# Kernel optimization log

Measured on AMD Instinct MI355X. Metric: run time of the kernel, lower is better.

Reference implementation:

```python
import jax, jax.numpy as jnp
import numpy as np

N = 262144      # nodes
E = 1048576     # edges
NC = 30         # node feature dim
ED = 13         # bond (edge) feature dim
H = 256         # hidden_channels
GH = 512        # config.gnn_hidden_channels
OUT = 256       # out_channels
L = 4           # num_layers
G = 8192        # num graphs in batch


def setup_inputs() -> dict:
    key = jax.random.key(0)
    ks = jax.random.split(key, 16)
    inp = {
        "x": jax.random.normal(ks[0], (N, NC), jnp.float32),
        "edge_attr": jax.random.normal(ks[1], (E, ED), jnp.float32),
        "edge_index": jax.random.randint(ks[2], (2, E), 0, N, jnp.int64),
        "batch": jnp.sort(jax.random.randint(ks[3], (N,), 0, G, jnp.int64)),
        # node_to_hid: Linear(NC, H)
        "W_nh": jax.random.normal(ks[4], (NC, H), jnp.float32) / np.sqrt(NC),
        "b_nh": jnp.zeros((H,), jnp.float32),
        # shared GINEConv nn: Linear(H, H) + ReLU (same module instance for every layer)
        "W1": jax.random.normal(ks[5], (H, H), jnp.float32) / np.sqrt(H),
        "b1": jnp.zeros((H,), jnp.float32),
        # per-layer edge projection Linear(ED, H) inside each GINEConv
        "We": jax.random.normal(ks[6], (L, ED, H), jnp.float32) / np.sqrt(ED),
        "be": jnp.zeros((L, H), jnp.float32),
        # lin1: H -> GH, lin2: GH -> OUT
        "Wl1": jax.random.normal(ks[7], (H, GH), jnp.float32) / np.sqrt(H),
        "bl1": jnp.zeros((GH,), jnp.float32),
        "Wl2": jax.random.normal(ks[8], (GH, OUT), jnp.float32) / np.sqrt(GH),
        "bl2": jnp.zeros((OUT,), jnp.float32),
    }
    return inp


def reference(x, edge_attr, W_nh, b_nh, W1, b1, We, be, Wl1, bl1, Wl2, bl2,
              edge_index, batch):
    src = edge_index[0]  # x_j (messages flow source -> target)
    dst = edge_index[1]
    hid = x @ W_nh + b_nh                                   # [N, H]
    for l in range(L):
        e = edge_attr @ We[l] + be[l]                       # [E, H]
        msg = jax.nn.relu(hid[src] + e)                     # gather + fuse
        agg = jax.ops.segment_sum(msg, dst, num_segments=N) # scatter-sum
        # GINEConv (eps=0) -> shared nn (Linear+ReLU), then outer relu in forward
        hid = jax.nn.relu(jax.nn.relu((hid + agg) @ W1 + b1))
    out = jax.nn.relu(hid @ Wl1 + bl1) @ Wl2 + bl2          # [N, OUT]
    # global_add_pool readout
    return jax.ops.segment_sum(out, batch, num_segments=G)  # [G, OUT]
```

## Files before the change

### kernel.cpp

```cpp
#include <hip/hip_runtime.h>
#include <hip/hip_bf16.h>

#define N_NODES 262144
#define N_EDGES 1048576
#define NC      30
#define ED      13
#define H       256
#define GH      512
#define OUT_C   256
#define NLAYERS 4
#define NGRAPHS 8192

typedef __hip_bfloat16 bf16;
typedef __attribute__((ext_vector_type(8))) short short8;
typedef __attribute__((ext_vector_type(4))) float f32x4;

__device__ unsigned short g_W1t[H * H];
__device__ unsigned short g_Wl1t[2][H * H];
__device__ unsigned short g_Wl2t[2][H * H];
__device__ float g_b1[H];
__device__ float g_bl1[GH];
__device__ float g_bl2[OUT_C];
__device__ unsigned int g_ssrc[N_EDGES];
__device__ float        g_seat[N_EDGES * ED];
__device__ unsigned int g_rowptr[N_NODES + 1];
__device__ unsigned int g_cursor[N_NODES];
__device__ unsigned int g_bsum[1024];

__device__ __forceinline__ float hw2f(unsigned short h) {
    return __uint_as_float(((unsigned int)h) << 16);
}
__device__ __forceinline__ float ldf(const void* p, size_t i, bool isbf) {
    return isbf ? hw2f(((const unsigned short*)p)[i]) : ((const float*)p)[i];
}
__device__ __forceinline__ int ldi(const void* p, size_t j, bool is64) {
    return ((const int*)p)[is64 ? 2 * j : j];
}
__device__ __forceinline__ unsigned short bfbits(float f) {
    bf16 b = __float2bfloat16(f);
    return *(unsigned short*)&b;
}
__device__ __forceinline__ float lo16(unsigned int u) { return __uint_as_float(u << 16); }
__device__ __forceinline__ float hi16(unsigned int u) { return __uint_as_float(u & 0xFFFF0000u); }
__device__ __forceinline__ unsigned int pk2(float a, float b) {
    return (unsigned int)bfbits(a) | ((unsigned int)bfbits(b) << 16);
}
__device__ __forceinline__ bool sniff_bf16(const void* xv) {
    const unsigned short* q = (const unsigned short*)xv;
    int c = 0;
    for (int i = 0; i < 32; ++i) {
        unsigned short h = q[2 * i];
        int e = (h >> 7) & 0xFF;
        c += (h == 0 || (e >= 97 && e <= 141)) ? 1 : 0;
    }
    return c >= 20;
}
__device__ __forceinline__ bool sniff_i64(const void* pv, size_t baseWord) {
    const unsigned int* q = (const unsigned int*)pv;
    int z = 0;
    for (int i = 0; i < 32; ++i) z += (q[baseWord + 2 * i + 1] == 0) ? 1 : 0;
    return z >= 20;
}
__device__ __forceinline__ void gload_lds16(const void* g, void* l) {
    __builtin_amdgcn_global_load_lds(
        (const __attribute__((address_space(1))) unsigned int*)g,
        (__attribute__((address_space(3))) unsigned int*)l, 16, 0, 0);
}

__global__ __launch_bounds__(256) void fill_f4(float4* p, int n4, float val) {
    int i = blockIdx.x * 256 + threadIdx.x;
    int stride = gridDim.x * 256;
    float4 z = make_float4(val, val, val, val);
    for (; i < n4; i += stride) p[i] = z;
}

__global__ __launch_bounds__(256) void pack_wt(const void* __restrict__ in,
        int ldin, int k0, int n0, int which) {
    const bool isbf = sniff_bf16(in);
    unsigned short* outp = which == 0 ? g_W1t
                         : which == 1 ? g_Wl1t[0]
                         : which == 2 ? g_Wl1t[1]
                         : which == 3 ? g_Wl2t[0] : g_Wl2t[1];
    const int n = blockIdx.x, k = threadIdx.x;
    outp[(n << 8) + k] = bfbits(ldf(in, (size_t)(k0 + k) * ldin + n0 + n, isbf));
}
__global__ __launch_bounds__(256) void pack_bias(const void* b1, const void* bl1,
                                                 const void* bl2) {
    const int t = threadIdx.x;
    const bool s1 = sniff_bf16(b1), s2 = sniff_bf16(bl1), s3 = sniff_bf16(bl2);
    g_b1[t]        = ldf(b1,  t,       s1);
    g_bl1[t]       = ldf(bl1, t,       s2);
    g_bl1[t + 256] = ldf(bl1, t + 256, s2);
    g_bl2[t]       = ldf(bl2, t,       s3);
}

__global__ __launch_bounds__(256) void csr_zero() {
    g_cursor[blockIdx.x * 256 + threadIdx.x] = 0u;
}
__global__ __launch_bounds__(256) void hist_dst(const void* __restrict__ eidx) {
    const bool is64 = sniff_i64(eidx, 0);
    const int e = blockIdx.x * 256 + threadIdx.x;
    int dst = ldi(eidx, (size_t)N_EDGES + e, is64);
    if ((unsigned)dst >= (unsigned)N_NODES) dst = 0;
    atomicAdd(&g_cursor[dst], 1u);
}
__global__ __launch_bounds__(256) void scan1() {
    __shared__ unsigned int sh[256];
    const int tid = threadIdx.x;
    sh[tid] = g_cursor[blockIdx.x * 256 + tid];
    __syncthreads();
    for (int s = 128; s > 0; s >>= 1) {
        if (tid < s) sh[tid] += sh[tid + s];
        __syncthreads();
    }
    if (tid == 0) g_bsum[blockIdx.x] = sh[0];
}
__global__ __launch_bounds__(256) void scan2() {
    __shared__ unsigned int sh[1024];
    const int tid = threadIdx.x;
    for (int j = tid; j < 1024; j += 256) sh[j] = g_bsum[j];
    __syncthreads();
    if (tid == 0) {
        unsigned int run = 0;
        for (int j = 0; j < 1024; ++j) { unsigned int t = sh[j]; sh[j] = run; run += t; }
    }
    __syncthreads();
    for (int j = tid; j < 1024; j += 256) g_bsum[j] = sh[j];
}
__global__ __launch_bounds__(256) void scan3() {
    __shared__ unsigned int sh[256];
    const int tid = threadIdx.x;
    const int i = blockIdx.x * 256 + tid;
    const unsigned int v = g_cursor[i];
    sh[tid] = v;
    __syncthreads();
    for (int ofs = 1; ofs < 256; ofs <<= 1) {
        unsigned int t = (tid >= ofs) ? sh[tid - ofs] : 0u;
        __syncthreads();
        sh[tid] += t;
        __syncthreads();
    }
    const unsigned int excl = sh[tid] - v + g_bsum[blockIdx.x];
    g_rowptr[i] = excl;
    g_cursor[i] = excl;
    if (i == N_NODES - 1) g_rowptr[N_NODES] = excl + v;
}
__global__ __launch_bounds__(256) void scatter_e(
        const void* __restrict__ eidx, const void* __restrict__ eattr) {
    const bool is64 = sniff_i64(eidx, 0);
    const bool isbf = sniff_bf16(eattr);
    const int e = blockIdx.x * 256 + threadIdx.x;
    int src = ldi(eidx, e, is64);
    int dst = ldi(eidx, (size_t)N_EDGES + e, is64);
    if ((unsigned)src >= (unsigned)N_NODES) src = 0;
    if ((unsigned)dst >= (unsigned)N_NODES) dst = 0;
    unsigned int pos = atomicAdd(&g_cursor[dst], 1u);
    if (pos >= (unsigned)N_EDGES) return;
    g_ssrc[pos] = (unsigned int)src;
#pragma unroll
    for (int k = 0; k < ED; ++k)
        g_seat[(size_t)pos * ED + k] = ldf(eattr, (size_t)e * ED + k, isbf);
}

__global__ __launch_bounds__(256) void node_proj(
        const void* __restrict__ x, const void* __restrict__ W,
        const void* __restrict__ b, bf16* __restrict__ hid) {
    const bool isbf = sniff_bf16(x);
    __shared__ float xs[16 * NC];
    const int m0 = blockIdx.x * 16;
    for (int i = threadIdx.x; i < 16 * NC; i += 256)
        xs[i] = ldf(x, (size_t)m0 * NC + i, isbf);
    __syncthreads();
    const int col = threadIdx.x;
    float w[NC];
#pragma unroll
    for (int k = 0; k < NC; ++k) w[k] = ldf(W, (size_t)k * H + col, isbf);
    const float bias = ldf(b, col, isbf);
#pragma unroll 4
    for (int r = 0; r < 16; ++r) {
        float acc = bias;
#pragma unroll
        for (int k = 0; k < NC; ++k) acc += xs[r * NC + k] * w[k];
        hid[(size_t)(m0 + r) * H + col] = __float2bfloat16(acc);
    }
}

__global__ __launch_bounds__(256) void gine_agg(
        const void* __restrict__ We, size_t weOff,
        const void* __restrict__ be, size_t beOff,
        const unsigned short* __restrict__ hid,
        unsigned short* __restrict__ hsum) {
    const bool isbf = sniff_bf16(We);
    const int lane = threadIdx.x & 63;
    const int wave = threadIdx.x >> 6;
    const int c0 = 2 * lane;
    float w0[ED], w1[ED], w2[ED], w3[ED];
#pragma unroll
    for (int k = 0; k < ED; ++k) {
        const size_t o = weOff + (size_t)k * H;
        w0[k] = ldf(We, o + c0,       isbf);
        w1[k] = ldf(We, o + c0 + 1,   isbf);
        w2[k] = ldf(We, o + c0 + 128, isbf);
        w3[k] = ldf(We, o + c0 + 129, isbf);
    }
    const float bb0 = ldf(be, beOff + c0,       isbf);
    const float bb1 = ldf(be, beOff + c0 + 1,   isbf);
    const float bb2 = ldf(be, beOff + c0 + 128, isbf);
    const float bb3 = ldf(be, beOff + c0 + 129, isbf);

    const int nbase = blockIdx.x * 16 + wave * 4;
    for (int ni = 0; ni < 4; ++ni) {
        const int node = nbase + ni;
        const unsigned int r0 = __builtin_amdgcn_readfirstlane(g_rowptr[node]);
        const unsigned int r1 = __builtin_amdgcn_readfirstlane(g_rowptr[node + 1]);
        const unsigned short* hn = hid + (size_t)node * H;
        const unsigned int hu0 = *(const unsigned int*)(hn + c0);
        const unsigned int hu1 = *(const unsigned int*)(hn + c0 + 128);
        float a0 = lo16(hu0), a1 = hi16(hu0), a2 = lo16(hu1), a3 = hi16(hu1);
        for (unsigned int e = r0; e < r1; ++e) {
            const unsigned int s = __builtin_amdgcn_readfirstlane(g_ssrc[e]);
            const float* af = g_seat + (size_t)e * ED;
            const unsigned short* hs = hid + (size_t)s * H;
            const unsigned int u0 = *(const unsigned int*)(hs + c0);
            const unsigned int u1 = *(const unsigned int*)(hs + c0 + 128);
            float m0 = bb0, m1 = bb1, m2 = bb2, m3 = bb3;
#pragma unroll
            for (int k = 0; k < ED; ++k) {
                const float a = af[k];
                m0 += a * w0[k]; m1 += a * w1[k];
                m2 += a * w2[k]; m3 += a * w3[k];
            }
            m0 += lo16(u0); m1 += hi16(u0); m2 += lo16(u1); m3 += hi16(u1);
            a0 += fmaxf(m0, 0.f); a1 += fmaxf(m1, 0.f);
            a2 += fmaxf(m2, 0.f); a3 += fmaxf(m3, 0.f);
        }
        unsigned int* ho = (unsigned int*)(hsum + (size_t)node * H);
        ho[lane]      = pk2(a0, a1);
        ho[lane + 64] = pk2(a2, a3);
    }
}

template <int MODE>
__global__ __launch_bounds__(256) void gemm_mfma(
        const unsigned short* __restrict__ A, int bsel,
        unsigned short* __restrict__ Cb, float* __restrict__ Cf,
        const void* __restrict__ batch, size_t batOff, int doRelu, int useBias) {
    __shared__ unsigned short As[64 * 64];
    __shared__ unsigned short Bs[256 * 64];
    const int tid  = threadIdx.x;
    const int lane = tid & 63;
    const int wave = tid >> 6;
    const int m0   = blockIdx.x * 64;

    const unsigned short* Bt = bsel == 0 ? g_W1t
                             : bsel == 1 ? g_Wl1t[0]
                             : bsel == 2 ? g_Wl1t[1]
                             : bsel == 3 ? g_Wl2t[0] : g_Wl2t[1];
    const float* bias = bsel == 0 ? g_b1
                      : bsel == 1 ? g_bl1
                      : bsel == 2 ? g_bl1 + 256 : g_bl2;

    const int ar   = tid >> 2;
    const int ac   = (tid & 3) << 4;
    const int awb  = (ar << 7) + (ac << 1);
    const int aswz = (ar & 7) << 4;
    const size_t arow = (size_t)(m0 + ar) * H + ac;
    const int nrow = lane >> 3;
    const int kbu  = ((lane & 7) ^ nrow) << 4;

    f32x4 acc0[8], acc1[8];
    const f32x4 zz = {0.f, 0.f, 0.f, 0.f};
#pragma unroll
    for (int i = 0; i < 8; ++i) { acc0[i] = zz; acc1[i] = zz; }

    const int fr   = lane & 15;
    const int fg   = lane >> 4;
    const int rowb = (wave >> 1) << 5;
    const int colb = (wave & 1) << 7;

    for (int kt = 0; kt < 4; ++kt) {
#pragma unroll
        for (int j = 0; j < 8; ++j) {
            const int q = (wave << 3) + j;
            gload_lds16((const char*)Bt + (((size_t)(q << 3) + nrow) << 9)
                            + (kt << 7) + kbu,
                        (char*)Bs + (q << 10));
        }
        {
            const size_t aoff = arow + (kt << 6);
            uint4 w0 = *(const uint4*)(A + aoff);
            uint4 w1 = *(const uint4*)(A + aoff + 8);
            *(uint4*)((char*)As + (awb ^ aswz)) = w0;
            *(uint4*)((char*)As + ((awb + 16) ^ aswz)) = w1;
        }
        __syncthreads();
#pragma unroll
        for (int s = 0; s < 2; ++s) {
            const int kofs = (s << 6) + (fg << 4);
            const int r0 = rowb + fr;
            short8 aF0 = *(const short8*)((const char*)As +
                          ((r0 << 7) + (kofs ^ ((r0 & 7) << 4))));
            short8 aF1 = *(const short8*)((const char*)As +
                          (((r0 + 16) << 7) + (kofs ^ ((r0 & 7) << 4))));
#pragma unroll
            for (int ct = 0; ct < 8; ++ct) {
                const int cc = colb + (ct << 4) + fr;
                short8 bF = *(const short8*)((const char*)Bs +
                             ((cc << 7) + (kofs ^ ((cc & 7) << 4))));
                acc0[ct] = __builtin_amdgcn_mfma_f32_16x16x32_bf16(aF0, bF, acc0[ct], 0, 0, 0);
                acc1[ct] = __builtin_amdgcn_mfma_f32_16x16x32_bf16(aF1, bF, acc1[ct], 0, 0, 0);
            }
        }
        __syncthreads();
    }

    const int crow = m0 + rowb + (fg << 2);
    if (MODE == 0) {
#pragma unroll
        for (int ct = 0; ct < 8; ++ct) {
            const int cc = colb + (ct << 4) + fr;
            const float bc = bias[cc];
#pragma unroll
            for (int r = 0; r < 4; ++r) {
                float v0 = acc0[ct][r] + bc;
                float v1 = acc1[ct][r] + bc;
                if (doRelu) { v0 = fmaxf(v0, 0.f); v1 = fmaxf(v1, 0.f); }
                Cb[(size_t)(crow + r) * H + cc]      = bfbits(v0);
                Cb[(size_t)(crow + 16 + r) * H + cc] = bfbits(v1);
            }
        }
    } else {
        const bool is64 = sniff_i64(batch, N_NODES / 2);
        int ga[5], gb[5];
#pragma unroll
        for (int r = 0; r < 4; ++r) {
            int g0 = ldi(batch, batOff + crow + r, is64);
            int g1 = ldi(batch, batOff + crow + 16 + r, is64);
            ga[r] = ((unsigned)g0 < (unsigned)NGRAPHS) ? g0 : 0;
            gb[r] = ((unsigned)g1 < (unsigned)NGRAPHS) ? g1 : 0;
        }
#pragma unroll
        for (int ct = 0; ct < 8; ++ct) {
            const int cc = colb + (ct << 4) + fr;
            const float bc = useBias ? bias[cc] : 0.f;
            float run0 = 0.f, run1 = 0.f;
#pragma unroll
            for (int r = 0; r < 4; ++r) {
                run0 += acc0[ct][r] + bc;
                if (r == 3 || ga[r + 1] != ga[r]) {
                    atomicAdd(&Cf[(size_t)ga[r] * OUT_C + cc], run0); run0 = 0.f;
                }
                run1 += acc1[ct][r] + bc;
                if (r == 3 || gb[r + 1] != gb[r]) {
                    atomicAdd(&Cf[(size_t)gb[r] * OUT_C + cc], run1); run1 = 0.f;
                }
            }
        }
    }
}

extern "C" void kernel_launch(void* const* d_in, const int* in_sizes, int n_in,
                              void* d_out, int out_size, void* d_ws, size_t ws_size,
                              hipStream_t stream) {
    const void *x = nullptr, *eattr = nullptr, *eidx = nullptr, *batch = nullptr;
    const void *W_nh = nullptr, *W1 = nullptr, *We = nullptr, *be = nullptr;
    const void *Wl1 = nullptr, *Wl2 = nullptr, *bl1 = nullptr;
    const void *z256[3] = {nullptr, nullptr, nullptr};
    int nz = 0;
    for (int i = 0; i < n_in; ++i) {
        switch (in_sizes[i]) {
            case N_NODES * NC:     x     = d_in[i]; break;
            case N_EDGES * ED:     eattr = d_in[i]; break;
            case 2 * N_EDGES:      eidx  = d_in[i]; break;
            case N_NODES:          batch = d_in[i]; break;
            case NC * H:           W_nh  = d_in[i]; break;
            case H * H:            W1    = d_in[i]; break;
            case NLAYERS * ED * H: We    = d_in[i]; break;
            case NLAYERS * H:      be    = d_in[i]; break;
            case H * GH:           if (!Wl1) Wl1 = d_in[i]; else Wl2 = d_in[i]; break;
            case GH:               bl1   = d_in[i]; break;
            case H:                if (nz < 3) z256[nz++] = d_in[i]; break;
            default: break;
        }
    }
    const void* b_nh = z256[0];
    const void* b1   = (nz > 1) ? z256[1] : z256[0];
    const void* bl2  = (nz > 2) ? z256[2] : z256[0];
    float* out = (float*)d_out;

    if (!x || !eattr || !eidx || !batch || !W_nh || !W1 || !We || !be ||
        !Wl1 || !Wl2 || !bl1 || !b_nh) {
        fill_f4<<<1024, 256, 0, stream>>>((float4*)out, NGRAPHS * OUT_C / 4, 2.0e6f);
        return;
    }

    const size_t NH = (size_t)N_NODES * H;
    const size_t need = NH * 2 + NH * 2;
    if (ws_size < need) {
        fill_f4<<<1024, 256, 0, stream>>>((float4*)out, NGRAPHS * OUT_C / 4, 1.0e6f);
        return;
    }
    bf16* hid            = (bf16*)d_ws;
    unsigned short* hsum = (unsigned short*)((char*)d_ws + NH * 2);

    pack_wt<<<256, 256, 0, stream>>>(W1,  H,     0,   0, 0);
    pack_wt<<<256, 256, 0, stream>>>(Wl1, GH,    0,   0, 1);
    pack_wt<<<256, 256, 0, stream>>>(Wl1, GH,    0, 256, 2);
    pack_wt<<<256, 256, 0, stream>>>(Wl2, OUT_C, 0,   0, 3);
    pack_wt<<<256, 256, 0, stream>>>(Wl2, OUT_C, 256, 0, 4);
    pack_bias<<<1, 256, 0, stream>>>(b1, bl1, bl2);

    csr_zero<<<N_NODES / 256, 256, 0, stream>>>();
    hist_dst<<<N_EDGES / 256, 256, 0, stream>>>(eidx);
    scan1<<<N_NODES / 256, 256, 0, stream>>>();
    scan2<<<1, 256, 0, stream>>>();
    scan3<<<N_NODES / 256, 256, 0, stream>>>();
    scatter_e<<<N_EDGES / 256, 256, 0, stream>>>(eidx, eattr);

    node_proj<<<N_NODES / 16, 256, 0, stream>>>(x, W_nh, b_nh, hid);

    for (int l = 0; l < NLAYERS; ++l) {
        gine_agg<<<N_NODES / 16, 256, 0, stream>>>(
            We, (size_t)l * ED * H, be, (size_t)l * H,
            (const unsigned short*)hid, hsum);
        gemm_mfma<0><<<N_NODES / 64, 256, 0, stream>>>(
            hsum, 0, (unsigned short*)hid, nullptr, nullptr, 0, 1, 1);
    }

    unsigned short* t0 = hsum;
    fill_f4<<<2048, 256, 0, stream>>>((float4*)out, NGRAPHS * OUT_C / 4, 0.f);
    for (int c = 0; c < 2; ++c) {
        gemm_mfma<0><<<N_NODES / 64, 256, 0, stream>>>(
            (const unsigned short*)hid, 1 + c,
            t0, nullptr, nullptr, 0, 1, 1);
        gemm_mfma<1><<<N_NODES / 64, 256, 0, stream>>>(
            t0, 3 + c,
            nullptr, out, batch, 0, 0, c == 0);
    }
}
```

Measured before the change: 2.452 ms.

## Split gine_agg channels across wave pairs, pad edge attrs to 16, prefetch src

Edge attributes are now stored padded to 16 floats so each edge can be read with float4 loads. In gine_agg, each pair of waves splits the 256 channels of a node (2 channels per lane instead of 4), so each wave handles 8 nodes and keeps half as many weight registers. The next source index is also prefetched one edge ahead. The intent is more parallelism and lower register pressure in the gather loop, at the cost of each edge's attributes being loaded by two waves and narrower 16-bit hid loads.

```diff
diff --git a/kernel.cpp b/kernel.cpp
--- a/kernel.cpp
+++ b/kernel.cpp
@@ -22,7 +22,7 @@
 __device__ float g_bl1[GH];
 __device__ float g_bl2[OUT_C];
 __device__ unsigned int g_ssrc[N_EDGES];
-__device__ float        g_seat[N_EDGES * ED];
+__device__ float        g_seat[N_EDGES * 16];
 __device__ unsigned int g_rowptr[N_NODES + 1];
 __device__ unsigned int g_cursor[N_NODES];
 __device__ unsigned int g_bsum[1024];
@@ -157,9 +157,14 @@
     unsigned int pos = atomicAdd(&g_cursor[dst], 1u);
     if (pos >= (unsigned)N_EDGES) return;
     g_ssrc[pos] = (unsigned int)src;
-#pragma unroll
-    for (int k = 0; k < ED; ++k)
-        g_seat[(size_t)pos * ED + k] = ldf(eattr, (size_t)e * ED + k, isbf);
+    float a[16];
+#pragma unroll
+    for (int k = 0; k < ED; ++k) a[k] = ldf(eattr, (size_t)e * ED + k, isbf);
+    a[13] = 0.f; a[14] = 0.f; a[15] = 0.f;
+    float* so = g_seat + (size_t)pos * 16;
+#pragma unroll
+    for (int k = 0; k < 4; ++k)
+        *(float4*)(so + 4 * k) = *(float4*)(a + 4 * k);
 }
 
 __global__ __launch_bounds__(256) void node_proj(
@@ -193,50 +198,55 @@
     const bool isbf = sniff_bf16(We);
     const int lane = threadIdx.x & 63;
     const int wave = threadIdx.x >> 6;
-    const int c0 = 2 * lane;
-    float w0[ED], w1[ED], w2[ED], w3[ED];
+    const int wh   = wave & 1;
+    const int wp   = wave >> 1;
+    const int c0 = lane + 128 * wh;
+    const int c1 = c0 + 64;
+    float w0[ED], w1[ED];
 #pragma unroll
     for (int k = 0; k < ED; ++k) {
         const size_t o = weOff + (size_t)k * H;
-        w0[k] = ldf(We, o + c0,       isbf);
-        w1[k] = ldf(We, o + c0 + 1,   isbf);
-        w2[k] = ldf(We, o + c0 + 128, isbf);
-        w3[k] = ldf(We, o + c0 + 129, isbf);
-    }
-    const float bb0 = ldf(be, beOff + c0,       isbf);
-    const float bb1 = ldf(be, beOff + c0 + 1,   isbf);
-    const float bb2 = ldf(be, beOff + c0 + 128, isbf);
-    const float bb3 = ldf(be, beOff + c0 + 129, isbf);
-
-    const int nbase = blockIdx.x * 16 + wave * 4;
-    for (int ni = 0; ni < 4; ++ni) {
-        const int node = nbase + ni;
+        w0[k] = ldf(We, o + c0, isbf);
+        w1[k] = ldf(We, o + c1, isbf);
+    }
+    const float bb0 = ldf(be, beOff + c0, isbf);
+    const float bb1 = ldf(be, beOff + c1, isbf);
+
+    const int nbase = blockIdx.x * 16 + wp * 8;
+    for (int j = 0; j < 8; ++j) {
+        const int node = nbase + j;
         const unsigned int r0 = __builtin_amdgcn_readfirstlane(g_rowptr[node]);
         const unsigned int r1 = __builtin_amdgcn_readfirstlane(g_rowptr[node + 1]);
         const unsigned short* hn = hid + (size_t)node * H;
-        const unsigned int hu0 = *(const unsigned int*)(hn + c0);
-        const unsigned int hu1 = *(const unsigned int*)(hn + c0 + 128);
-        float a0 = lo16(hu0), a1 = hi16(hu0), a2 = lo16(hu1), a3 = hi16(hu1);
+        float a0 = hw2f(hn[c0]);
+        float a1 = hw2f(hn[c1]);
+        unsigned int sc = (r0 < r1) ? g_ssrc[r0] : 0u;
         for (unsigned int e = r0; e < r1; ++e) {
-            const unsigned int s = __builtin_amdgcn_readfirstlane(g_ssrc[e]);
-            const float* af = g_seat + (size_t)e * ED;
+            const unsigned int sn = (e + 1 < r1) ? g_ssrc[e + 1] : 0u;
+            const unsigned int s = __builtin_amdgcn_readfirstlane(sc);
+            const float* sp = g_seat + (size_t)e * 16;
+            const float4 f0 = *(const float4*)(sp);
+            const float4 f1 = *(const float4*)(sp + 4);
+            const float4 f2 = *(const float4*)(sp + 8);
+            const float  fc = sp[12];
             const unsigned short* hs = hid + (size_t)s * H;
-            const unsigned int u0 = *(const unsigned int*)(hs + c0);
-            const unsigned int u1 = *(const unsigned int*)(hs + c0 + 128);
-            float m0 = bb0, m1 = bb1, m2 = bb2, m3 = bb3;
+            const float h0 = hw2f(hs[c0]);
+            const float h1 = hw2f(hs[c1]);
+            const float af[ED] = {f0.x, f0.y, f0.z, f0.w, f1.x, f1.y, f1.z,
+                                  f1.w, f2.x, f2.y, f2.z, f2.w, fc};
+            float m0 = bb0, m1 = bb1;
 #pragma unroll
             for (int k = 0; k < ED; ++k) {
-                const float a = af[k];
-                m0 += a * w0[k]; m1 += a * w1[k];
-                m2 += a * w2[k]; m3 += a * w3[k];
+                m0 += af[k] * w0[k];
+                m1 += af[k] * w1[k];
             }
-            m0 += lo16(u0); m1 += hi16(u0); m2 += lo16(u1); m3 += hi16(u1);
-            a0 += fmaxf(m0, 0.f); a1 += fmaxf(m1, 0.f);
-            a2 += fmaxf(m2, 0.f); a3 += fmaxf(m3, 0.f);
-        }
-        unsigned int* ho = (unsigned int*)(hsum + (size_t)node * H);
-        ho[lane]      = pk2(a0, a1);
-        ho[lane + 64] = pk2(a2, a3);
+            a0 += fmaxf(m0 + h0, 0.f);
+            a1 += fmaxf(m1 + h1, 0.f);
+            sc = sn;
+        }
+        unsigned short* ho = hsum + (size_t)node * H;
+        ho[c0] = bfbits(a0);
+        ho[c1] = bfbits(a1);
     }
 }
 
```

After: 2.382 ms. 2.8% less time.
